# Kernel optimization log

Hardware: AMD Instinct MI355X
Metric: run time of the kernel (lower is better)

## Reference

```python
import jax, jax.numpy as jnp
import numpy as np

B, S, H = 2, 2048, 4096
NUM_HEADS = 32
HEAD_DIM = H // NUM_HEADS  # 128
ROPE_BASE = 10000.0


def _apply_rope(x, positions):
    # x: [B, S, nh, hd]; neox-style (half-split) rotation, rotary_dim == head_dim
    hd = x.shape[-1]
    inv_freq = 1.0 / (ROPE_BASE ** (jnp.arange(0, hd, 2, dtype=jnp.float32) / hd))  # [hd/2]
    freqs = positions[..., None].astype(jnp.float32) * inv_freq  # [B, S, hd/2]
    cos = jnp.cos(freqs)[:, :, None, :].astype(x.dtype)
    sin = jnp.sin(freqs)[:, :, None, :].astype(x.dtype)
    x1, x2 = jnp.split(x, 2, axis=-1)
    return jnp.concatenate([x1 * cos - x2 * sin, x2 * cos + x1 * sin], axis=-1)


def setup_inputs() -> dict:
    key = jax.random.key(0)
    k1, k2, k3 = jax.random.split(key, 3)
    hidden_states = jax.random.normal(k1, (B, S, H), dtype=jnp.float32) * 0.02
    positions = jnp.broadcast_to(jnp.arange(S, dtype=jnp.int32), (B, S))
    w_pack = jax.random.normal(k2, (3 * H, H), dtype=jnp.float32) * 0.02  # Linear(H, 3H), no bias
    w_o = jax.random.normal(k3, (H, H), dtype=jnp.float32) * 0.02        # Linear(H, H), no bias
    return {"hidden_states": hidden_states, "w_pack": w_pack, "w_o": w_o, "positions": positions}


def reference(hidden_states, w_pack, w_o, positions):
    b, s, h = hidden_states.shape
    nh, hd = NUM_HEADS, HEAD_DIM
    # fused QKV projection (W_pack)
    qkv = hidden_states @ w_pack.T  # [B, S, 3H]
    q, k, v = jnp.split(qkv, 3, axis=-1)
    q = q.reshape(b, s, nh, hd)
    k = k.reshape(b, s, nh, hd)
    v = v.reshape(b, s, nh, hd)
    # RoPE on q and k
    q = _apply_rope(q, positions)
    k = _apply_rope(k, positions)
    # causal scaled-dot-product attention (prefill over full KV cache)
    scale = 1.0 / jnp.sqrt(jnp.asarray(hd, dtype=q.dtype))
    scores = jnp.einsum('bqhd,bkhd->bhqk', q, k) * scale  # [B, nh, S, S]
    causal = jnp.tril(jnp.ones((s, s), dtype=bool))
    neg = jnp.asarray(jnp.finfo(scores.dtype).min, dtype=scores.dtype)
    scores = jnp.where(causal[None, None], scores, neg)
    attn = jax.nn.softmax(scores, axis=-1)
    out = jnp.einsum('bhqk,bkhd->bqhd', attn, v).reshape(b, s, h)
    # output projection
    return out @ w_o.T
```

## Files before the change

kernel.cpp:

```cpp
#include <hip/hip_runtime.h>
#include <hip/hip_bf16.h>
#include <math.h>

#define B_    2
#define S_    2048
#define H_    4096
#define NH_   32
#define HD_   128
#define MTOK_ (B_ * S_)
#define QKVN_ (3 * H_)

using bf16_t = __hip_bfloat16;
typedef __bf16 bf16x8 __attribute__((ext_vector_type(8)));
typedef unsigned short u16x8 __attribute__((ext_vector_type(8)));
typedef float f32x4 __attribute__((ext_vector_type(4)));

#define ASYNC_COPY16(g, l)                                                     \
  __builtin_amdgcn_global_load_lds(                                            \
      (__attribute__((address_space(1))) void*)(g),                            \
      (__attribute__((address_space(3))) void*)(l), 16, 0, 0)

static __device__ __forceinline__ f32x4 mfma16x16(bf16x8 a, bf16x8 b, f32x4 c) {
  return __builtin_amdgcn_mfma_f32_16x16x32_bf16(a, b, c, 0, 0, 0);
}

static __device__ __forceinline__ float bits_to_f(unsigned short v) {
  union { unsigned int u; float f; } cv;
  cv.u = ((unsigned int)v) << 16;
  return cv.f;
}

__global__ void bh_detect(const unsigned short* __restrict__ p,
                          int* __restrict__ flag) {
  __shared__ float red[4];
  float m = 0.f;
  const int tid = threadIdx.x;
  for (int i = tid; i < 65536; i += 256) {
    const float f = fabsf(bits_to_f(p[i]));
    m = fmaxf(m, f);
  }
  for (int off = 1; off < 64; off <<= 1) m = fmaxf(m, __shfl_xor(m, off, 64));
  if ((tid & 63) == 0) red[tid >> 6] = m;
  __syncthreads();
  if (tid == 0) {
    const float mm = fmaxf(fmaxf(red[0], red[1]), fmaxf(red[2], red[3]));
    *flag = (mm > 1.0f) ? 1 : 0;
  }
}

__global__ __launch_bounds__(256)
void bh_convert(const void* __restrict__ src, bf16_t* __restrict__ dst,
                long n8, const int* __restrict__ flag) {
  const int isf = *flag;
  const long stride = (long)gridDim.x * 256;
  long i = (long)blockIdx.x * 256 + threadIdx.x;
  if (isf) {
    const f32x4* s = (const f32x4*)src;
    for (; i < n8; i += stride) {
      const f32x4 f0 = s[2 * i];
      const f32x4 f1 = s[2 * i + 1];
      bf16x8 o;
      o[0] = (__bf16)f0[0]; o[1] = (__bf16)f0[1];
      o[2] = (__bf16)f0[2]; o[3] = (__bf16)f0[3];
      o[4] = (__bf16)f1[0]; o[5] = (__bf16)f1[1];
      o[6] = (__bf16)f1[2]; o[7] = (__bf16)f1[3];
      *reinterpret_cast<bf16x8*>(dst + i * 8) = o;
    }
  } else {
    const u16x8* s = (const u16x8*)src;
    for (; i < n8; i += stride)
      reinterpret_cast<u16x8*>(dst)[i] = s[i];
  }
}

static __device__ __forceinline__ void stage32(const float* __restrict__ g,
                                               bf16_t* __restrict__ l) {
  const f32x4 f0 = *reinterpret_cast<const f32x4*>(g);
  const f32x4 f1 = *reinterpret_cast<const f32x4*>(g + 4);
  bf16x8 o;
  o[0] = (__bf16)f0[0]; o[1] = (__bf16)f0[1];
  o[2] = (__bf16)f0[2]; o[3] = (__bf16)f0[3];
  o[4] = (__bf16)f1[0]; o[5] = (__bf16)f1[1];
  o[6] = (__bf16)f1[2]; o[7] = (__bf16)f1[3];
  *reinterpret_cast<bf16x8*>(l) = o;
}

template <int AMODE, int BMODE, int CMODE>
__global__ __launch_bounds__(256, 2)
void bh_gemm(const void* __restrict__ Ap, int lda,
             const void* __restrict__ Bp, int ldb,
             void* __restrict__ Cp, int ldc, int N, int K,
             const int* __restrict__ flag) {
  __shared__ bf16_t As[128 * 32];
  __shared__ bf16_t Bs[128 * 32];
  const int isf = *flag;
  const bool a_f32 = AMODE && isf;
  const bool b_f32 = BMODE && isf;

  const int tid = threadIdx.x, wave = tid >> 6, lane = tid & 63;
  const int lq = lane >> 4, lc = lane & 15;
  const int m0 = blockIdx.y * 128, n0 = blockIdx.x * 128;
  const int wm = (wave >> 1) * 64, wn = (wave & 1) * 64;

  f32x4 acc[4][4] = {};

  const int srow  = wave * 16 + (lane >> 2);
  const int skoff = (lane & 3) * 8;

  const bf16_t* a16 = (const bf16_t*)Ap;
  const float*  a32 = (const float*)Ap;
  const bf16_t* b16 = (const bf16_t*)Bp;
  const float*  b32 = (const float*)Bp;

  bf16_t* lA0u = As + wave * 512;
  bf16_t* lA1u = As + 2048 + wave * 512;
  bf16_t* lB0u = Bs + wave * 512;
  bf16_t* lB1u = Bs + 2048 + wave * 512;
  bf16_t* lA0p = lA0u + lane * 8;
  bf16_t* lA1p = lA1u + lane * 8;
  bf16_t* lB0p = lB0u + lane * 8;
  bf16_t* lB1p = lB1u + lane * 8;

  const int aoff = (wm + lc) * 32 + lq * 8;
  const int boff = (wn + lc) * 32 + lq * 8;

  for (int k = 0; k < K; k += 32) {
    if (a_f32) {
      stage32(a32 + (long)(m0 + srow) * lda + skoff + k, lA0p);
      stage32(a32 + (long)(m0 + srow + 64) * lda + skoff + k, lA1p);
    } else {
      ASYNC_COPY16(a16 + (long)(m0 + srow) * lda + skoff + k, lA0u);
      ASYNC_COPY16(a16 + (long)(m0 + srow + 64) * lda + skoff + k, lA1u);
    }
    if (b_f32) {
      stage32(b32 + (long)(n0 + srow) * ldb + skoff + k, lB0p);
      stage32(b32 + (long)(n0 + srow + 64) * ldb + skoff + k, lB1p);
    } else {
      ASYNC_COPY16(b16 + (long)(n0 + srow) * ldb + skoff + k, lB0u);
      ASYNC_COPY16(b16 + (long)(n0 + srow + 64) * ldb + skoff + k, lB1u);
    }
    __syncthreads();
    bf16x8 af[4], bfr[4];
#pragma unroll
    for (int i = 0; i < 4; ++i) {
      af[i]  = *reinterpret_cast<const bf16x8*>(&As[aoff + i * 512]);
      bfr[i] = *reinterpret_cast<const bf16x8*>(&Bs[boff + i * 512]);
    }
#pragma unroll
    for (int mi = 0; mi < 4; ++mi)
#pragma unroll
      for (int ni = 0; ni < 4; ++ni)
        acc[mi][ni] = mfma16x16(af[mi], bfr[ni], acc[mi][ni]);
    __syncthreads();
  }

  const bool c_f32 = CMODE && isf;
#pragma unroll
  for (int mi = 0; mi < 4; ++mi)
#pragma unroll
    for (int ni = 0; ni < 4; ++ni)
#pragma unroll
      for (int i = 0; i < 4; ++i) {
        const long row = m0 + wm + mi * 16 + lq * 4 + i;
        const long col = n0 + wn + ni * 16 + lc;
        const float v = acc[mi][ni][i];
        if (c_f32)
          ((float*)Cp)[row * ldc + col] = v;
        else
          ((bf16_t*)Cp)[row * ldc + col] = __float2bfloat16(v);
      }
}

#define GBAR()                                                                 \
  do {                                                                         \
    __builtin_amdgcn_s_barrier();                                              \
    __builtin_amdgcn_sched_barrier(0);                                         \
  } while (0)

#define LGKM0()                                                                \
  do {                                                                         \
    asm volatile("s_waitcnt lgkmcnt(0)" ::: "memory");                         \
    __builtin_amdgcn_sched_barrier(0);                                         \
  } while (0)

template <int CMODE>
__global__ __launch_bounds__(512, 2)
void bh_gemm2(const bf16_t* __restrict__ Ap, int lda,
              const bf16_t* __restrict__ Bp, int ldb,
              void* __restrict__ Cp, int ldc, int K,
              const int* __restrict__ flag) {
  __shared__ bf16_t As[2][2][128 * 64];
  __shared__ bf16_t Bs[2][2][128 * 64];
  const int isf = *flag;

  const int tid = threadIdx.x, wave = tid >> 6, lane = tid & 63;
  const int lq = lane >> 4, lc = lane & 15;
  const int wm2 = wave >> 2;
  const int wn4 = wave & 3;
  const int m0 = blockIdx.y * 256, n0 = blockIdx.x * 256;
  const int NT = K >> 6;

  const int srow = wave * 16 + (lane >> 3);
  const int gcol = ((lane & 7) ^ (lane >> 3)) * 8;
  const int lbase = wave * 1024;

  f32x4 acc[8][4] = {};
  bf16x8 aA[2][4];
  bf16x8 bB[2][2][2];

  auto stageA = [&](int tau, int h) {
    if (tau >= NT) return;
    const bf16_t* g = Ap + (long)(m0 + h * 128 + srow) * lda + tau * 64 + gcol;
    bf16_t* l = &As[tau & 1][h][lbase];
    ASYNC_COPY16(g, l);
    ASYNC_COPY16(g + (long)8 * lda, l + 512);
  };
  auto stageB = [&](int tau, int h) {
    if (tau >= NT) return;
    const bf16_t* g = Bp + (long)(n0 + h * 128 + srow) * ldb + tau * 64 + gcol;
    bf16_t* l = &Bs[tau & 1][h][lbase];
    ASYNC_COPY16(g, l);
    ASYNC_COPY16(g + (long)8 * ldb, l + 512);
  };
  auto ldA = [&](int buf, int h) {
#pragma unroll
    for (int ks = 0; ks < 2; ++ks)
#pragma unroll
      for (int f = 0; f < 4; ++f) {
        const int row = wm2 * 64 + f * 16 + lc;
        aA[ks][f] = *reinterpret_cast<const bf16x8*>(
            &As[buf][h][row * 64 + (((ks * 4 + lq) ^ (row & 7)) * 8)]);
      }
  };
  auto ldB = [&](int buf, int h, bf16x8 (&dst)[2][2]) {
#pragma unroll
    for (int ks = 0; ks < 2; ++ks)
#pragma unroll
      for (int g = 0; g < 2; ++g) {
        const int row = wn4 * 32 + g * 16 + lc;
        dst[ks][g] = *reinterpret_cast<const bf16x8*>(
            &Bs[buf][h][row * 64 + (((ks * 4 + lq) ^ (row & 7)) * 8)]);
      }
  };

#define MMA_QUAD(qm, qn)                                                       \
  do {                                                                         \
    __builtin_amdgcn_s_setprio(1);                                             \
    _Pragma("unroll") for (int f = 0; f < 4; ++f) {                            \
      _Pragma("unroll") for (int g = 0; g < 2; ++g) {                          \
        f32x4 c = acc[(qm) * 4 + f][(qn) * 2 + g];                             \
        c = mfma16x16(aA[0][f], bB[qn][0][g], c);                              \
        c = mfma16x16(aA[1][f], bB[qn][1][g], c);                              \
        acc[(qm) * 4 + f][(qn) * 2 + g] = c;                                   \
      }                                                                        \
    }                                                                          \
    __builtin_amdgcn_s_setprio(0);                                             \
  } while (0)

  stageA(0, 0); stageB(0, 0); stageB(0, 1); stageA(0, 1);
  stageA(1, 0); stageB(1, 0); stageB(1, 1);
  asm volatile("s_waitcnt vmcnt(6)" ::: "memory");
  GBAR();

  for (int T = 0; T < NT; ++T) {
    const int buf = T & 1;
    ldA(buf, 0);
    ldB(buf, 0, bB[0]);
    stageA(T + 1, 1);
    asm volatile("s_waitcnt lgkmcnt(8)" ::: "memory");
    GBAR();
    LGKM0();
    MMA_QUAD(0, 0);
    GBAR();
    ldB(buf, 1, bB[1]);
    stageA(T + 2, 0);
    GBAR();
    LGKM0();
    MMA_QUAD(0, 1);
    GBAR();
    ldA(buf, 1);
    stageB(T + 2, 0);
    GBAR();
    LGKM0();
    MMA_QUAD(1, 1);
    GBAR();
    stageB(T + 2, 1);
    if (T + 2 < NT)
      asm volatile("s_waitcnt vmcnt(6)" ::: "memory");
    else
      asm volatile("s_waitcnt vmcnt(0)" ::: "memory");
    GBAR();
    MMA_QUAD(1, 0);
    GBAR();
  }

  const bool c_f32 = CMODE && isf;
#pragma unroll
  for (int mi = 0; mi < 8; ++mi)
#pragma unroll
    for (int ni = 0; ni < 4; ++ni)
#pragma unroll
      for (int i = 0; i < 4; ++i) {
        const long row =
            m0 + (mi >> 2) * 128 + wm2 * 64 + (mi & 3) * 16 + lq * 4 + i;
        const long col =
            n0 + (ni >> 1) * 128 + wn4 * 32 + (ni & 1) * 16 + lc;
        const float v = acc[mi][ni][i];
        if (c_f32)
          ((float*)Cp)[row * ldc + col] = v;
        else
          ((bf16_t*)Cp)[row * ldc + col] = __float2bfloat16(v);
      }
}

__global__ void bh_rope(bf16_t* __restrict__ qkv, const int* __restrict__ pos) {
  const int idx = blockIdx.x * 256 + threadIdx.x;
  const int d = idx & 63;
  const int h = (idx >> 6) & (NH_ - 1);
  const int m = idx >> 11;
  if (m >= MTOK_) return;
  const float p = (float)pos[m];
  const float inv_freq = 1.0f / powf(10000.0f, (float)d * (1.0f / 64.0f));
  float sn, cs;
  sincosf(p * inv_freq, &sn, &cs);
  bf16_t* q  = qkv + (long)m * QKVN_ + h * HD_;
  bf16_t* kk = q + H_;
  const float q1 = __bfloat162float(q[d]);
  const float q2 = __bfloat162float(q[d + 64]);
  q[d]      = __float2bfloat16(q1 * cs - q2 * sn);
  q[d + 64] = __float2bfloat16(q2 * cs + q1 * sn);
  const float k1 = __bfloat162float(kk[d]);
  const float k2 = __bfloat162float(kk[d + 64]);
  kk[d]      = __float2bfloat16(k1 * cs - k2 * sn);
  kk[d + 64] = __float2bfloat16(k2 * cs + k1 * sn);
}

__global__ void bh_transpose_v(const bf16_t* __restrict__ qkv,
                               bf16_t* __restrict__ vt) {
  __shared__ unsigned short tile[128][65];
  const int t0 = blockIdx.x * 64;
  const int h  = blockIdx.y;
  const int b  = blockIdx.z;
  const int tid = threadIdx.x;
#pragma unroll
  for (int pass = 0; pass < 4; ++pass) {
    const int row = (tid >> 4) + pass * 16;
    const int dc  = (tid & 15) * 8;
    const u16x8 v = *reinterpret_cast<const u16x8*>(
        qkv + (long)(b * S_ + t0 + row) * QKVN_ + 2 * H_ + h * HD_ + dc);
#pragma unroll
    for (int j = 0; j < 8; ++j) tile[dc + j][row] = v[j];
  }
  __syncthreads();
#pragma unroll
  for (int pass = 0; pass < 4; ++pass) {
    const int d  = (tid >> 3) + pass * 32;
    const int tc = (tid & 7) * 8;
    u16x8 o;
#pragma unroll
    for (int j = 0; j < 8; ++j) o[j] = tile[d][tc + j];
    *reinterpret_cast<u16x8*>(
        vt + ((long)(b * NH_ + h) * HD_ + d) * S_ + t0 + tc) = o;
  }
}

__global__ __launch_bounds__(256)
void bh_flash(bf16_t* __restrict__ qkv, const bf16_t* __restrict__ vt) {
  __shared__ bf16_t Ks[64 * 128];
  __shared__ bf16_t Vs[128 * 64];
  __shared__ bf16_t Ps[128 * 64];
  const int qt = blockIdx.x, h = blockIdx.y, b = blockIdx.z;
  const int tid = threadIdx.x, wave = tid >> 6, lane = tid & 63;
  const int lq = lane >> 4, lc = lane & 15;
  const int wrow = wave * 32;
  const float scale = 0.088388347648318447f;

  bf16x8 qf[2][4];
#pragma unroll
  for (int mt = 0; mt < 2; ++mt) {
    const bf16_t* qp =
        qkv + (long)(b * S_ + qt * 128 + wrow + mt * 16 + lc) * QKVN_ +
        h * HD_ + lq * 8;
#pragma unroll
    for (int ks = 0; ks < 4; ++ks)
      qf[mt][ks] = *reinterpret_cast<const bf16x8*>(qp + ks * 32);
  }

  f32x4 o_acc[2][8] = {};
  float m_st[2][4], l_st[2][4];
#pragma unroll
  for (int mt = 0; mt < 2; ++mt)
#pragma unroll
    for (int i = 0; i < 4; ++i) { m_st[mt][i] = -1e30f; l_st[mt][i] = 0.f; }

  const int ktiles = 2 * qt + 2;
  for (int kt = 0; kt < ktiles; ++kt) {
    const int t0 = kt * 64;
#pragma unroll
    for (int j = 0; j < 4; ++j) {
      const int p = wave * 4 + j;
      const int trow = p * 4 + (lane >> 4);
      const int kcs  = ((lane & 15) ^ (trow & 7)) * 8;
      ASYNC_COPY16(qkv + (long)(b * S_ + t0 + trow) * QKVN_ + H_ + h * HD_ + kcs,
                   Ks + p * 512);
      const int vrow = p * 8 + (lane >> 3);
      const int tcs  = ((lane & 7) ^ (lane >> 3)) * 8;
      ASYNC_COPY16(vt + ((long)(b * NH_ + h) * HD_ + vrow) * S_ + t0 + tcs,
                   Vs + p * 512);
    }
    __syncthreads();

    f32x4 sa[2][4] = {};
#pragma unroll
    for (int ks = 0; ks < 4; ++ks) {
      bf16x8 bb[4];
#pragma unroll
      for (int nt = 0; nt < 4; ++nt)
        bb[nt] = *reinterpret_cast<const bf16x8*>(
            &Ks[(nt * 16 + lc) * 128 + ((ks * 32 + lq * 8) ^ ((lc & 7) << 3))]);
#pragma unroll
      for (int mt = 0; mt < 2; ++mt)
#pragma unroll
        for (int nt = 0; nt < 4; ++nt)
          sa[mt][nt] = mfma16x16(qf[mt][ks], bb[nt], sa[mt][nt]);
    }

#pragma unroll
    for (int mt = 0; mt < 2; ++mt) {
#pragma unroll
      for (int i = 0; i < 4; ++i) {
        const int qg = qt * 128 + wrow + mt * 16 + lq * 4 + i;
        float sv[4];
        float mloc = -1e30f;
#pragma unroll
        for (int nt = 0; nt < 4; ++nt) {
          float v = sa[mt][nt][i] * scale;
          if (t0 + nt * 16 + lc > qg) v = -1e30f;
          sv[nt] = v;
          mloc = fmaxf(mloc, v);
        }
#pragma unroll
        for (int off = 1; off < 16; off <<= 1)
          mloc = fmaxf(mloc, __shfl_xor(mloc, off, 64));
        const float mnew = fmaxf(m_st[mt][i], mloc);
        const float alpha = __expf(m_st[mt][i] - mnew);
        float rsum = 0.f;
        const int psw = ((lq * 4 + i) & 7) << 3;
#pragma unroll
        for (int nt = 0; nt < 4; ++nt) {
          const float pp = __expf(sv[nt] - mnew);
          rsum += pp;
          Ps[(wrow + mt * 16 + lq * 4 + i) * 64 + ((nt * 16 + lc) ^ psw)] =
              __float2bfloat16(pp);
        }
#pragma unroll
        for (int off = 1; off < 16; off <<= 1)
          rsum += __shfl_xor(rsum, off, 64);
        l_st[mt][i] = l_st[mt][i] * alpha + rsum;
        m_st[mt][i] = mnew;
#pragma unroll
        for (int nt = 0; nt < 8; ++nt) o_acc[mt][nt][i] *= alpha;
      }
    }
    __syncthreads();

#pragma unroll
    for (int ks = 0; ks < 2; ++ks) {
      bf16x8 pa[2];
#pragma unroll
      for (int mt = 0; mt < 2; ++mt)
        pa[mt] = *reinterpret_cast<const bf16x8*>(
            &Ps[(wrow + mt * 16 + lc) * 64 +
                ((ks * 32 + lq * 8) ^ ((lc & 7) << 3))]);
#pragma unroll
      for (int nt = 0; nt < 8; ++nt) {
        const bf16x8 vb = *reinterpret_cast<const bf16x8*>(
            &Vs[(nt * 16 + lc) * 64 +
                ((ks * 32 + lq * 8) ^ ((lc & 7) << 3))]);
#pragma unroll
        for (int mt = 0; mt < 2; ++mt)
          o_acc[mt][nt] = mfma16x16(pa[mt], vb, o_acc[mt][nt]);
      }
    }
    __syncthreads();
  }

#pragma unroll
  for (int mt = 0; mt < 2; ++mt)
#pragma unroll
    for (int i = 0; i < 4; ++i) {
      const float inv_l = 1.0f / l_st[mt][i];
      bf16_t* op =
          qkv + (long)(b * S_ + qt * 128 + wrow + mt * 16 + lq * 4 + i) * QKVN_ +
          h * HD_ + lc;
#pragma unroll
      for (int nt = 0; nt < 8; ++nt)
        op[nt * 16] = __float2bfloat16(o_acc[mt][nt][i] * inv_l);
    }
}

extern "C" void kernel_launch(void* const* d_in, const int* in_sizes, int n_in,
                              void* d_out, int out_size, void* d_ws,
                              size_t ws_size, hipStream_t stream) {
  const int* pos = (const int*)d_in[3];

  char* ws = (char*)d_ws;
  bf16_t* qkv  = (bf16_t*)ws;
  const size_t QKV_B = (size_t)MTOK_ * QKVN_ * 2;
  int*    flag = (int*)(ws + QKV_B);
  bf16_t* vt   = (bf16_t*)d_out;

  const size_t off  = QKV_B + 512;
  const size_t WP_B = (size_t)QKVN_ * H_ * 2;
  const size_t WO_B = (size_t)H_ * H_ * 2;
  const size_t A_B  = (size_t)MTOK_ * H_ * 2;
  const bool cvtWP = ws_size >= off + WP_B;
  const bool cvtWO = ws_size >= off + WP_B + WO_B;
  const bool cvtA  = ws_size >= off + WP_B + WO_B + A_B;
  bf16_t* wpb = (bf16_t*)(ws + off);
  bf16_t* wob = (bf16_t*)(ws + off + WP_B);
  bf16_t* abf = (bf16_t*)(ws + off + WP_B + WO_B);

  bh_detect<<<dim3(1), dim3(256), 0, stream>>>(
      (const unsigned short*)d_in[1], flag);

  if (cvtWP)
    bh_convert<<<dim3(2048), dim3(256), 0, stream>>>(
        d_in[1], wpb, (long)QKVN_ * H_ / 8, flag);
  if (cvtWO)
    bh_convert<<<dim3(2048), dim3(256), 0, stream>>>(
        d_in[2], wob, (long)H_ * H_ / 8, flag);
  if (cvtA)
    bh_convert<<<dim3(2048), dim3(256), 0, stream>>>(
        d_in[0], abf, (long)MTOK_ * H_ / 8, flag);

  if (cvtA)
    bh_gemm2<0><<<dim3(QKVN_ / 256, MTOK_ / 256), dim3(512), 0, stream>>>(
        abf, H_, wpb, H_, qkv, QKVN_, H_, flag);
  else if (cvtWP)
    bh_gemm<1, 0, 0><<<dim3(QKVN_ / 128, MTOK_ / 128), dim3(256), 0, stream>>>(
        d_in[0], H_, wpb, H_, qkv, QKVN_, QKVN_, H_, flag);
  else
    bh_gemm<1, 1, 0><<<dim3(QKVN_ / 128, MTOK_ / 128), dim3(256), 0, stream>>>(
        d_in[0], H_, d_in[1], H_, qkv, QKVN_, QKVN_, H_, flag);

  bh_rope<<<dim3((MTOK_ * NH_ * 64) / 256), dim3(256), 0, stream>>>(qkv, pos);
  bh_transpose_v<<<dim3(S_ / 64, NH_, B_), dim3(256), 0, stream>>>(qkv, vt);
  bh_flash<<<dim3(S_ / 128, NH_, B_), dim3(256), 0, stream>>>(qkv, vt);

  if (cvtWO)
    bh_gemm2<1><<<dim3(H_ / 256, MTOK_ / 256), dim3(512), 0, stream>>>(
        qkv, QKVN_, wob, H_, d_out, H_, H_, flag);
  else
    bh_gemm<0, 1, 1><<<dim3(H_ / 128, MTOK_ / 128), dim3(256), 0, stream>>>(
        qkv, QKVN_, d_in[2], H_, d_out, H_, H_, H_, flag);
}
```

Before: 1.410 ms.

## Double-buffer K/V tiles in flash attention and schedule heavy query tiles first

The flash attention kernel now keeps two LDS buffers for K and V. It prefetches the next key tile with async global-to-LDS copies while computing on the current one, and waits on vmcnt instead of a full barrier. The grid is flattened so the largest causal query tiles launch first, which improves load balance. s_setprio is raised around the MFMA sections, and the barrier between softmax and PV is dropped because each wave only reads its own rows of P. The cost is doubled LDS use for K/V, which may lower occupancy.

```diff
diff --git a/kernel.cpp b/kernel.cpp
--- a/kernel.cpp
+++ b/kernel.cpp
@@ -29,6 +29,18 @@
   cv.u = ((unsigned int)v) << 16;
   return cv.f;
 }
+
+#define GBAR()                                                                 \
+  do {                                                                         \
+    __builtin_amdgcn_s_barrier();                                              \
+    __builtin_amdgcn_sched_barrier(0);                                         \
+  } while (0)
+
+#define LGKM0()                                                                \
+  do {                                                                         \
+    asm volatile("s_waitcnt lgkmcnt(0)" ::: "memory");                         \
+    __builtin_amdgcn_sched_barrier(0);                                         \
+  } while (0)
 
 __global__ void bh_detect(const unsigned short* __restrict__ p,
                           int* __restrict__ flag) {
@@ -170,18 +182,6 @@
           ((bf16_t*)Cp)[row * ldc + col] = __float2bfloat16(v);
       }
 }
-
-#define GBAR()                                                                 \
-  do {                                                                         \
-    __builtin_amdgcn_s_barrier();                                              \
-    __builtin_amdgcn_sched_barrier(0);                                         \
-  } while (0)
-
-#define LGKM0()                                                                \
-  do {                                                                         \
-    asm volatile("s_waitcnt lgkmcnt(0)" ::: "memory");                         \
-    __builtin_amdgcn_sched_barrier(0);                                         \
-  } while (0)
 
 template <int CMODE>
 __global__ __launch_bounds__(512, 2)
@@ -366,10 +366,14 @@
 
 __global__ __launch_bounds__(256)
 void bh_flash(bf16_t* __restrict__ qkv, const bf16_t* __restrict__ vt) {
-  __shared__ bf16_t Ks[64 * 128];
-  __shared__ bf16_t Vs[128 * 64];
+  __shared__ bf16_t Ks[2][64 * 128];
+  __shared__ bf16_t Vs[2][128 * 64];
   __shared__ bf16_t Ps[128 * 64];
-  const int qt = blockIdx.x, h = blockIdx.y, b = blockIdx.z;
+  const int idx = blockIdx.x;
+  const int qt = (S_ / 128 - 1) - (idx >> 6);
+  const int bh = idx & 63;
+  const int b  = bh >> 5;
+  const int h  = bh & (NH_ - 1);
   const int tid = threadIdx.x, wave = tid >> 6, lane = tid & 63;
   const int lq = lane >> 4, lc = lane & 15;
   const int wrow = wave * 32;
@@ -393,8 +397,7 @@
 #pragma unroll
     for (int i = 0; i < 4; ++i) { m_st[mt][i] = -1e30f; l_st[mt][i] = 0.f; }
 
-  const int ktiles = 2 * qt + 2;
-  for (int kt = 0; kt < ktiles; ++kt) {
+  auto stage = [&](int kt, int bsel) {
     const int t0 = kt * 64;
 #pragma unroll
     for (int j = 0; j < 4; ++j) {
@@ -402,28 +405,45 @@
       const int trow = p * 4 + (lane >> 4);
       const int kcs  = ((lane & 15) ^ (trow & 7)) * 8;
       ASYNC_COPY16(qkv + (long)(b * S_ + t0 + trow) * QKVN_ + H_ + h * HD_ + kcs,
-                   Ks + p * 512);
+                   &Ks[bsel][p * 512]);
       const int vrow = p * 8 + (lane >> 3);
       const int tcs  = ((lane & 7) ^ (lane >> 3)) * 8;
       ASYNC_COPY16(vt + ((long)(b * NH_ + h) * HD_ + vrow) * S_ + t0 + tcs,
-                   Vs + p * 512);
-    }
-    __syncthreads();
-
+                   &Vs[bsel][p * 512]);
+    }
+  };
+
+  const int ktiles = 2 * qt + 2;
+  stage(0, 0);
+
+  for (int kt = 0; kt < ktiles; ++kt) {
+    const int cur = kt & 1;
+    if (kt + 1 < ktiles) {
+      stage(kt + 1, cur ^ 1);
+      asm volatile("s_waitcnt vmcnt(8)" ::: "memory");
+    } else {
+      asm volatile("s_waitcnt vmcnt(0)" ::: "memory");
+    }
+    GBAR();
+
+    const int t0 = kt * 64;
     f32x4 sa[2][4] = {};
+    __builtin_amdgcn_s_setprio(1);
 #pragma unroll
     for (int ks = 0; ks < 4; ++ks) {
       bf16x8 bb[4];
 #pragma unroll
       for (int nt = 0; nt < 4; ++nt)
         bb[nt] = *reinterpret_cast<const bf16x8*>(
-            &Ks[(nt * 16 + lc) * 128 + ((ks * 32 + lq * 8) ^ ((lc & 7) << 3))]);
+            &Ks[cur][(nt * 16 + lc) * 128 +
+                     ((ks * 32 + lq * 8) ^ ((lc & 7) << 3))]);
 #pragma unroll
       for (int mt = 0; mt < 2; ++mt)
 #pragma unroll
         for (int nt = 0; nt < 4; ++nt)
           sa[mt][nt] = mfma16x16(qf[mt][ks], bb[nt], sa[mt][nt]);
     }
+    __builtin_amdgcn_s_setprio(0);
 
 #pragma unroll
     for (int mt = 0; mt < 2; ++mt) {
@@ -462,8 +482,8 @@
         for (int nt = 0; nt < 8; ++nt) o_acc[mt][nt][i] *= alpha;
       }
     }
-    __syncthreads();
-
+
+    __builtin_amdgcn_s_setprio(1);
 #pragma unroll
     for (int ks = 0; ks < 2; ++ks) {
       bf16x8 pa[2];
@@ -475,14 +495,15 @@
 #pragma unroll
       for (int nt = 0; nt < 8; ++nt) {
         const bf16x8 vb = *reinterpret_cast<const bf16x8*>(
-            &Vs[(nt * 16 + lc) * 64 +
-                ((ks * 32 + lq * 8) ^ ((lc & 7) << 3))]);
+            &Vs[cur][(nt * 16 + lc) * 64 +
+                     ((ks * 32 + lq * 8) ^ ((lc & 7) << 3))]);
 #pragma unroll
         for (int mt = 0; mt < 2; ++mt)
           o_acc[mt][nt] = mfma16x16(pa[mt], vb, o_acc[mt][nt]);
       }
     }
-    __syncthreads();
+    __builtin_amdgcn_s_setprio(0);
+    GBAR();
   }
 
 #pragma unroll
@@ -546,7 +567,7 @@
 
   bh_rope<<<dim3((MTOK_ * NH_ * 64) / 256), dim3(256), 0, stream>>>(qkv, pos);
   bh_transpose_v<<<dim3(S_ / 64, NH_, B_), dim3(256), 0, stream>>>(qkv, vt);
-  bh_flash<<<dim3(S_ / 128, NH_, B_), dim3(256), 0, stream>>>(qkv, vt);
+  bh_flash<<<dim3((S_ / 128) * NH_ * B_), dim3(256), 0, stream>>>(qkv, vt);
 
   if (cvtWO)
     bh_gemm2<1><<<dim3(H_ / 256, MTOK_ / 256), dim3(512), 0, stream>>>(
```

Result: faster. 1.166 ms (-17.3%).
